# Kernel optimization log

Hardware: AMD Instinct MI355X
Metric: run time of the kernel (lower is better)

The kernel has to match this reference:

```python
import jax, jax.numpy as jnp
import numpy as np

D_IN, D_H, BATCH = 4096, 512, 8192


def _layernorm(x, g, b, eps=1e-5):
    mu = jnp.mean(x, axis=-1, keepdims=True)
    var = jnp.var(x, axis=-1, keepdims=True)
    return (x - mu) * jax.lax.rsqrt(var + eps) * g + b


def setup_inputs() -> dict:
    key = jax.random.key(0)
    ks = jax.random.split(key, 10)
    x = jax.random.normal(ks[0], (BATCH, D_IN), jnp.float32)
    h = jax.random.normal(ks[1], (BATCH, D_H), jnp.float32)
    s1 = 1.0 / np.sqrt(D_IN + D_H)
    W1 = jax.random.uniform(ks[2], (D_IN + D_H, D_H), jnp.float32, -s1, s1)
    b1 = jnp.zeros((D_H,), jnp.float32)
    ln1_g = jnp.ones((D_H,), jnp.float32)
    ln1_b = jnp.zeros((D_H,), jnp.float32)
    s2 = 1.0 / np.sqrt(D_H)
    W2 = jax.random.uniform(ks[3], (D_H, 3 * D_H), jnp.float32, -s2, s2)
    b2 = jnp.zeros((3 * D_H,), jnp.float32)
    base_tau = jnp.ones((D_H,), jnp.float32)  # time_constant_init = 1.0
    base_A = jax.random.normal(ks[4], (D_H, D_H), jnp.float32) * 0.1
    idx = jnp.arange(D_H)
    base_A = base_A.at[idx, idx].set(-0.5)
    base_B = jax.random.normal(ks[5], (D_IN, D_H), jnp.float32) * 0.1
    hn_g = jnp.ones((D_H,), jnp.float32)
    hn_b = jnp.zeros((D_H,), jnp.float32)
    return {"x": x, "h": h, "W1": W1, "b1": b1, "ln1_g": ln1_g, "ln1_b": ln1_b,
            "W2": W2, "b2": b2, "base_tau": base_tau, "base_A": base_A,
            "base_B": base_B, "hn_g": hn_g, "hn_b": hn_b}


def reference(x, h, W1, b1, ln1_g, ln1_b, W2, b2, base_tau, base_A, base_B, hn_g, hn_b):
    dt = 0.1
    # time_net hypernetwork
    xh = jnp.concatenate([x, h], axis=-1)                 # [B, D_IN+D_H]
    t = _layernorm(xh @ W1 + b1, ln1_g, ln1_b)
    t = jax.nn.gelu(t, approximate=False)
    params = t @ W2 + b2                                  # [B, 3*D_H]
    tau_s, A_s, B_s = jnp.split(params, 3, axis=-1)
    tau = base_tau * (jax.nn.sigmoid(tau_s) * 2.0)        # [B, D_H]
    A_row = 1.0 + 0.5 * jnp.tanh(A_s)                     # per-sample row scale of A
    B_col = 1.0 + 0.5 * jnp.tanh(B_s)                     # per-sample col scale of B
    # A[b] = base_A * A_row[b][:,None]; h @ A[b].T == (h @ base_A.T) * A_row[b]
    recurrent = (h @ base_A.T) * A_row                    # [B, D_H]
    # B[b] = base_B * B_col[b][None,:]; x @ B[b] == (x @ base_B) * B_col[b]
    input_term = (x @ base_B) * B_col                     # [B, D_H]
    dhdt = -h / (tau + 1e-8) + jnp.tanh(recurrent + input_term)
    new_h = _layernorm(h + dt * dhdt, hn_g, hn_b)
    return new_h
```

## Files before the change

kernel.cpp:

```cpp
#include <hip/hip_runtime.h>

#define BATCH 8192
#define DIN 4096
#define DH 512

typedef float f32x4 __attribute__((ext_vector_type(4)));
typedef float f32x2 __attribute__((ext_vector_type(2)));
typedef short s16x8 __attribute__((ext_vector_type(8)));
typedef unsigned short u16x2 __attribute__((ext_vector_type(2)));
typedef unsigned short u16x4 __attribute__((ext_vector_type(4)));
typedef unsigned short u16x8 __attribute__((ext_vector_type(8)));

static __device__ __forceinline__ unsigned short f2bf(float f) {
  unsigned int u = __float_as_uint(f);
  u += 0x7FFFu + ((u >> 16) & 1u);
  return (unsigned short)(u >> 16);
}
static __device__ __forceinline__ float bf2f(unsigned short s) {
  return __uint_as_float(((unsigned int)s) << 16);
}

typedef const __attribute__((address_space(1))) unsigned int* gas_ptr;
typedef __attribute__((address_space(3))) unsigned int* las_ptr;
static __device__ __forceinline__ void gl_lds16(const unsigned short* g, unsigned short* l) {
  __builtin_amdgcn_global_load_lds((gas_ptr)g, (las_ptr)l, 16, 0, 0);
}

__global__ __launch_bounds__(256) void cast_bf16_k(
    const float* __restrict__ in, unsigned short* __restrict__ out)
{
  const int i = (blockIdx.x * 256 + threadIdx.x) * 4;
  f32x4 v = *(const f32x4*)(in + i);
  u16x4 p = { f2bf(v[0]), f2bf(v[1]), f2bf(v[2]), f2bf(v[3]) };
  *(u16x4*)(out + i) = p;
}

__global__ __launch_bounds__(256) void transpose_bf16_k(
    const float* __restrict__ in, int R, int C,
    unsigned short* __restrict__ out, int ldo, int row_off)
{
  __shared__ float tl[32][33];
  const int tx = threadIdx.x, ty = threadIdx.y;
  const int c0 = blockIdx.x * 32, r0 = blockIdx.y * 32;
#pragma unroll
  for (int i = 0; i < 4; i++)
    tl[ty + 8 * i][tx] = in[(size_t)(r0 + ty + 8 * i) * C + c0 + tx];
  __syncthreads();
#pragma unroll
  for (int i = 0; i < 4; i++)
    out[(size_t)(row_off + c0 + ty + 8 * i) * ldo + r0 + tx] = f2bf(tl[tx][ty + 8 * i]);
}

__global__ __launch_bounds__(256) void zfill_k(
    unsigned short* __restrict__ base, int ld, int rows, int cols8)
{
  const int gid = blockIdx.x * 256 + threadIdx.x;
  const int row = gid / cols8;
  const int c = (gid % cols8) * 8;
  if (row < rows) {
    u16x8 z = { 0, 0, 0, 0, 0, 0, 0, 0 };
    *(u16x8*)(base + (size_t)row * ld + c) = z;
  }
}

template<int EPI>
static __device__ __forceinline__ void gemm_engine(
    const unsigned short* __restrict__ A0, int lda0, int K0,
    const unsigned short* __restrict__ A1, int lda1,
    const unsigned short* __restrict__ BT, int ldb,
    unsigned short* __restrict__ C0, int ldc,
    unsigned short* __restrict__ C1,
    const float* __restrict__ bias,
    const float* __restrict__ base_tau,
    int mb, int nb, int K,
    unsigned short* As, unsigned short* Bs)
{
  const int tid = threadIdx.x;
  const int lane = tid & 63;
  const int wid = tid >> 6;
  const int wm = (wid >> 1) * 64;
  const int wn = (wid & 1) * 64;
  const int srow = lane >> 2;
  const int scol = (lane & 3) * 8;
  const int fr = lane & 15;
  const int fk = (lane >> 4) * 8;
  const int NT = K / 32;

  f32x4 acc[4][4];
#pragma unroll
  for (int i = 0; i < 4; i++)
#pragma unroll
    for (int j = 0; j < 4; j++)
      acc[i][j] = (f32x4){ 0.f, 0.f, 0.f, 0.f };

  auto STAGE = [&](int buf, int t) {
    const int k0 = t * 32;
    const bool s0 = (k0 < K0);
    const unsigned short* Ab = s0 ? A0 : A1;
    const int ld = s0 ? lda0 : lda1;
    const int ko = (s0 ? k0 : k0 - K0) + scol;
    unsigned short* ab = As + buf * 4096 + (32 * wid) * 32;
    unsigned short* bb = Bs + buf * 4096 + (32 * wid) * 32;
#pragma unroll
    for (int c = 0; c < 2; c++) {
      const int r = 32 * wid + c * 16 + srow;
      gl_lds16(Ab + (size_t)(mb + r) * ld + ko, ab + c * 16 * 32);
      gl_lds16(BT + (size_t)(nb + r) * ldb + k0 + scol, bb + c * 16 * 32);
    }
  };

  STAGE(0, 0);
  STAGE(1, 1);
  asm volatile("s_waitcnt vmcnt(4)" ::: "memory");
  __builtin_amdgcn_s_barrier();

  int cur = 0, stg = 2;
  for (int t = 0; t < NT; t++) {
    if (t + 2 < NT) STAGE(stg, t + 2);

    const unsigned short* ar = As + cur * 4096;
    const unsigned short* br = Bs + cur * 4096;
    s16x8 af[4], bv[4];
#pragma unroll
    for (int mi = 0; mi < 4; mi++)
      af[mi] = *(const s16x8*)(ar + (wm + mi * 16 + fr) * 32 + fk);
#pragma unroll
    for (int ni = 0; ni < 4; ni++)
      bv[ni] = *(const s16x8*)(br + (wn + ni * 16 + fr) * 32 + fk);

    asm volatile("s_waitcnt lgkmcnt(0)" ::: "memory");
    __builtin_amdgcn_sched_barrier(0);

#pragma unroll
    for (int mi = 0; mi < 4; mi++)
#pragma unroll
      for (int ni = 0; ni < 4; ni++)
        acc[mi][ni] = __builtin_amdgcn_mfma_f32_16x16x32_bf16(
            af[mi], bv[ni], acc[mi][ni], 0, 0, 0);

    if (t + 1 < NT) {
      if (t + 2 < NT) asm volatile("s_waitcnt vmcnt(4)" ::: "memory");
      else            asm volatile("s_waitcnt vmcnt(0)" ::: "memory");
      __builtin_amdgcn_s_barrier();
    }
    cur = (cur == 2) ? 0 : cur + 1;
    stg = (stg == 2) ? 0 : stg + 1;
  }

  const int rb = (lane >> 4) * 4;
#pragma unroll
  for (int mi = 0; mi < 4; mi++) {
#pragma unroll
    for (int ni = 0; ni < 4; ni++) {
#pragma unroll
      for (int r = 0; r < 4; r++) {
        const int row = mb + wm + mi * 16 + rb + r;
        const int col = nb + wn + ni * 16 + fr;
        float v = acc[mi][ni][r];
        if (EPI == 3) {
          if (col < DH) C0[(size_t)row * DH + col] = f2bf(v + bias[col]);
          else          C1[(size_t)row * DH + (col - DH)] = f2bf(v);
        } else if (EPI == 2) {
          C0[(size_t)row * ldc + col] = f2bf(v);
        } else if (EPI == 1) {
          v += bias[col];
          if ((col >> 9) == 0) {
            const float s = 1.0f / (1.0f + expf(-v));
            v = 1.0f / (base_tau[col & (DH - 1)] * 2.0f * s + 1e-8f);
          } else {
            v = 1.0f + 0.5f * tanhf(v);
          }
          C0[(size_t)row * ldc + col] = f2bf(v);
        }
      }
    }
  }
}

__global__ __launch_bounds__(256) void fused_gemm_k(
    const unsigned short* __restrict__ xbf,
    const unsigned short* __restrict__ hbf,
    const unsigned short* __restrict__ BTcat,
    unsigned short* __restrict__ pre1,
    unsigned short* __restrict__ rawB,
    const float* __restrict__ b1)
{
  __shared__ unsigned short As[3 * 4096];
  __shared__ unsigned short Bs[3 * 4096];
  const int cpx = gridDim.x >> 3;
  const int virt = (blockIdx.x & 7) * cpx + (blockIdx.x >> 3);
  const int mb = (virt & 63) * 128;
  const int nb = (virt >> 6) * 128;
  gemm_engine<3>(xbf, DIN, DIN, hbf, DH, BTcat, DIN + DH,
                 pre1, DH, rawB, b1, nullptr, mb, nb, DIN + DH, As, Bs);
}

__global__ __launch_bounds__(256) void tail_gemm_k(
    const unsigned short* __restrict__ hbf,
    const unsigned short* __restrict__ Abf,
    const unsigned short* __restrict__ tbf,
    const unsigned short* __restrict__ W2T,
    unsigned short* __restrict__ rawA,
    unsigned short* __restrict__ scales,
    const float* __restrict__ b2,
    const float* __restrict__ base_tau)
{
  __shared__ unsigned short As[3 * 4096];
  __shared__ unsigned short Bs[3 * 4096];
  const int b = blockIdx.x;
  if (b < 768) {
    const int mb = (b & 63) * 128, nb = (b >> 6) * 128;
    gemm_engine<1>(tbf, DH, DH, nullptr, 0, W2T, DH,
                   scales, 3 * DH, nullptr, b2, base_tau, mb, nb, DH, As, Bs);
  } else {
    const int b2i = b - 768;
    const int mb = (b2i & 63) * 128, nb = (b2i >> 6) * 128;
    gemm_engine<2>(hbf, DH, DH, nullptr, 0, Abf, DH,
                   rawA, DH, nullptr, nullptr, nullptr, mb, nb, DH, As, Bs);
  }
}

__device__ __forceinline__ float block_sum256(float v, float* red) {
#pragma unroll
  for (int m = 32; m >= 1; m >>= 1) v += __shfl_xor(v, m, 64);
  __syncthreads();
  if ((threadIdx.x & 63) == 0) red[threadIdx.x >> 6] = v;
  __syncthreads();
  return red[0] + red[1] + red[2] + red[3];
}

__global__ __launch_bounds__(256) void ln_gelu_k(
    const unsigned short* __restrict__ pre,
    const float* __restrict__ g, const float* __restrict__ b,
    unsigned short* __restrict__ t)
{
  __shared__ float red[4];
  const int row = blockIdx.x;
  const int c = threadIdx.x * 2;
  const size_t ro = (size_t)row * DH;
  u16x2 raw = *(const u16x2*)(pre + ro + c);
  const float v0 = bf2f(raw[0]), v1 = bf2f(raw[1]);
  const float mu = block_sum256(v0 + v1, red) * (1.0f / DH);
  const float d0 = v0 - mu, d1 = v1 - mu;
  const float var = block_sum256(d0 * d0 + d1 * d1, red) * (1.0f / DH);
  const float inv = rsqrtf(var + 1e-5f);
  const float y0 = d0 * inv * g[c] + b[c];
  const float y1 = d1 * inv * g[c + 1] + b[c + 1];
  u16x2 o = { f2bf(0.5f * y0 * (1.0f + erff(y0 * 0.70710678118f))),
              f2bf(0.5f * y1 * (1.0f + erff(y1 * 0.70710678118f))) };
  *(u16x2*)(t + ro + c) = o;
}

__global__ __launch_bounds__(256) void final_k(
    const float* __restrict__ h,
    const unsigned short* __restrict__ rawA,
    const unsigned short* __restrict__ rawB,
    const unsigned short* __restrict__ scales,
    const float* __restrict__ hn_g, const float* __restrict__ hn_b,
    float* __restrict__ out)
{
  __shared__ float red[4];
  const int row = blockIdx.x;
  const int c = threadIdx.x * 2;
  const size_t ro = (size_t)row * DH;
  f32x2 hv = *(const f32x2*)(h + ro + c);
  u16x2 ra = *(const u16x2*)(rawA + ro + c);
  u16x2 rb = *(const u16x2*)(rawB + ro + c);
  const unsigned short* sc = scales + (size_t)row * (3 * DH);
  u16x2 ti  = *(const u16x2*)(sc + c);
  u16x2 arw = *(const u16x2*)(sc + DH + c);
  u16x2 bcl = *(const u16x2*)(sc + 2 * DH + c);
  const float u0 = hv[0] + 0.1f * (-hv[0] * bf2f(ti[0])
                 + tanhf(bf2f(ra[0]) * bf2f(arw[0]) + bf2f(rb[0]) * bf2f(bcl[0])));
  const float u1 = hv[1] + 0.1f * (-hv[1] * bf2f(ti[1])
                 + tanhf(bf2f(ra[1]) * bf2f(arw[1]) + bf2f(rb[1]) * bf2f(bcl[1])));
  const float mu = block_sum256(u0 + u1, red) * (1.0f / DH);
  const float d0 = u0 - mu, d1 = u1 - mu;
  const float var = block_sum256(d0 * d0 + d1 * d1, red) * (1.0f / DH);
  const float inv = rsqrtf(var + 1e-5f);
  f32x2 o = { d0 * inv * hn_g[c] + hn_b[c],
              d1 * inv * hn_g[c + 1] + hn_b[c + 1] };
  *(f32x2*)(out + ro + c) = o;
}

extern "C" void kernel_launch(void* const* d_in, const int* in_sizes, int n_in,
                              void* d_out, int out_size, void* d_ws, size_t ws_size,
                              hipStream_t stream)
{
  const float* x        = (const float*)d_in[0];
  const float* h        = (const float*)d_in[1];
  const float* W1       = (const float*)d_in[2];
  const float* b1       = (const float*)d_in[3];
  const float* ln1_g    = (const float*)d_in[4];
  const float* ln1_b    = (const float*)d_in[5];
  const float* W2       = (const float*)d_in[6];
  const float* b2       = (const float*)d_in[7];
  const float* base_tau = (const float*)d_in[8];
  const float* base_A   = (const float*)d_in[9];
  const float* base_B   = (const float*)d_in[10];
  const float* hn_g     = (const float*)d_in[11];
  const float* hn_b     = (const float*)d_in[12];

  const int KC = DIN + DH;
  char* w = (char*)d_ws;
  unsigned short* xbf    = (unsigned short*)(w);
  unsigned short* hbf    = (unsigned short*)(w + 67108864);
  unsigned short* BTcat  = (unsigned short*)(w + 75497472);
  unsigned short* tbf    = (unsigned short*)(w + 75497472);
  unsigned short* W2T    = (unsigned short*)(w + 84934656);
  unsigned short* Abf    = (unsigned short*)(w + 86507520);
  unsigned short* pre1   = (unsigned short*)(w + 87031808);
  unsigned short* rawA   = (unsigned short*)(w + 87031808);
  unsigned short* rawB   = (unsigned short*)(w + 95420416);
  unsigned short* scales = (unsigned short*)(w + 103809024);

  cast_bf16_k<<<DIN * BATCH / 1024, 256, 0, stream>>>(x, xbf);
  cast_bf16_k<<<DH * BATCH / 1024, 256, 0, stream>>>(h, hbf);
  cast_bf16_k<<<DH * DH / 1024, 256, 0, stream>>>(base_A, Abf);
  dim3 tb(32, 8);
  transpose_bf16_k<<<dim3(DH / 32, KC / 32), tb, 0, stream>>>(W1, KC, DH, BTcat, KC, 0);
  transpose_bf16_k<<<dim3(DH / 32, DIN / 32), tb, 0, stream>>>(base_B, DIN, DH, BTcat, KC, DH);
  zfill_k<<<128, 256, 0, stream>>>(BTcat + (size_t)DH * KC + DIN, KC, DH, DH / 8);
  transpose_bf16_k<<<dim3(3 * DH / 32, DH / 32), tb, 0, stream>>>(W2, DH, 3 * DH, W2T, DH, 0);

  fused_gemm_k<<<512, 256, 0, stream>>>(xbf, hbf, BTcat, pre1, rawB, b1);
  ln_gelu_k<<<BATCH, 256, 0, stream>>>(pre1, ln1_g, ln1_b, tbf);
  tail_gemm_k<<<1024, 256, 0, stream>>>(hbf, Abf, tbf, W2T, rawA, scales, b2, base_tau);
  final_k<<<BATCH, 256, 0, stream>>>(h, rawA, rawB, scales, hn_g, hn_b, (float*)d_out);
}
```

Baseline: 242.0 us.

## Deepen main GEMM pipeline to four stages and merge prep kernels into one launch

The main fused GEMM now keeps four LDS stages in flight instead of three. Its wait counts are generalised so up to two stages stay outstanding while compute runs, which should hide more global-load latency. Six small preprocessing launches (h cast, base_A cast, three transposes, zero fill) are merged into a single block-indexed kernel to cut launch overhead and tail gaps. The extra stage raises LDS per block to 64KB, which may lower occupancy.

After: 236.3 us. 2.4% less time.

```diff
diff --git a/kernel.cpp b/kernel.cpp
--- a/kernel.cpp
+++ b/kernel.cpp
@@ -35,13 +35,14 @@
   *(u16x4*)(out + i) = p;
 }
 
-__global__ __launch_bounds__(256) void transpose_bf16_k(
-    const float* __restrict__ in, int R, int C,
-    unsigned short* __restrict__ out, int ldo, int row_off)
-{
-  __shared__ float tl[32][33];
-  const int tx = threadIdx.x, ty = threadIdx.y;
-  const int c0 = blockIdx.x * 32, r0 = blockIdx.y * 32;
+static __device__ __forceinline__ void transpose_body(
+    const float* __restrict__ in, int C,
+    unsigned short* __restrict__ out, int ldo, int row_off,
+    int bx, int by, float (*tl)[33])
+{
+  const int tid = threadIdx.x;
+  const int tx = tid & 31, ty = tid >> 5;
+  const int c0 = bx * 32, r0 = by * 32;
 #pragma unroll
   for (int i = 0; i < 4; i++)
     tl[ty + 8 * i][tx] = in[(size_t)(r0 + ty + 8 * i) * C + c0 + tx];
@@ -51,19 +52,45 @@
     out[(size_t)(row_off + c0 + ty + 8 * i) * ldo + r0 + tx] = f2bf(tl[tx][ty + 8 * i]);
 }
 
-__global__ __launch_bounds__(256) void zfill_k(
-    unsigned short* __restrict__ base, int ld, int rows, int cols8)
-{
-  const int gid = blockIdx.x * 256 + threadIdx.x;
-  const int row = gid / cols8;
-  const int c = (gid % cols8) * 8;
-  if (row < rows) {
+__global__ __launch_bounds__(256) void prep_small_k(
+    const float* __restrict__ h, unsigned short* __restrict__ hbf,
+    const float* __restrict__ base_A, unsigned short* __restrict__ Abf,
+    const float* __restrict__ W1, const float* __restrict__ base_B,
+    unsigned short* __restrict__ BTcat,
+    const float* __restrict__ W2, unsigned short* __restrict__ W2T)
+{
+  __shared__ float tl[32][33];
+  const int b = blockIdx.x;
+  const int tid = threadIdx.x;
+  const int KC = DIN + DH;
+  if (b < 4096) {
+    const int i = (b * 256 + tid) * 4;
+    f32x4 v = *(const f32x4*)(h + i);
+    u16x4 p = { f2bf(v[0]), f2bf(v[1]), f2bf(v[2]), f2bf(v[3]) };
+    *(u16x4*)(hbf + i) = p;
+  } else if (b < 4352) {
+    const int i = ((b - 4096) * 256 + tid) * 4;
+    f32x4 v = *(const f32x4*)(base_A + i);
+    u16x4 p = { f2bf(v[0]), f2bf(v[1]), f2bf(v[2]), f2bf(v[3]) };
+    *(u16x4*)(Abf + i) = p;
+  } else if (b < 6656) {
+    const int bb = b - 4352;
+    transpose_body(W1, DH, BTcat, KC, 0, bb & 15, bb >> 4, tl);
+  } else if (b < 8704) {
+    const int bb = b - 6656;
+    transpose_body(base_B, DH, BTcat, KC, DH, bb & 15, bb >> 4, tl);
+  } else if (b < 8832) {
+    const int gid = (b - 8704) * 256 + tid;
+    const int row = gid >> 6, c = (gid & 63) * 8;
     u16x8 z = { 0, 0, 0, 0, 0, 0, 0, 0 };
-    *(u16x8*)(base + (size_t)row * ld + c) = z;
+    *(u16x8*)(BTcat + (size_t)(DH + row) * KC + DIN + c) = z;
+  } else {
+    const int bb = b - 8832;
+    transpose_body(W2, 3 * DH, W2T, DH, 0, bb % 48, bb / 48, tl);
   }
 }
 
-template<int EPI>
+template<int EPI, int DEPTH>
 static __device__ __forceinline__ void gemm_engine(
     const unsigned short* __restrict__ A0, int lda0, int K0,
     const unsigned short* __restrict__ A1, int lda1,
@@ -109,17 +136,17 @@
     }
   };
 
-  STAGE(0, 0);
-  STAGE(1, 1);
-  asm volatile("s_waitcnt vmcnt(4)" ::: "memory");
+#pragma unroll
+  for (int d = 0; d < DEPTH - 1; d++) STAGE(d, d);
+  if (DEPTH == 4) asm volatile("s_waitcnt vmcnt(8)" ::: "memory");
+  else            asm volatile("s_waitcnt vmcnt(4)" ::: "memory");
   __builtin_amdgcn_s_barrier();
 
-  int cur = 0, stg = 2;
   for (int t = 0; t < NT; t++) {
-    if (t + 2 < NT) STAGE(stg, t + 2);
-
-    const unsigned short* ar = As + cur * 4096;
-    const unsigned short* br = Bs + cur * 4096;
+    if (t + DEPTH - 1 < NT) STAGE((t + DEPTH - 1) % DEPTH, t + DEPTH - 1);
+
+    const unsigned short* ar = As + (t % DEPTH) * 4096;
+    const unsigned short* br = Bs + (t % DEPTH) * 4096;
     s16x8 af[4], bv[4];
 #pragma unroll
     for (int mi = 0; mi < 4; mi++)
@@ -139,12 +166,13 @@
             af[mi], bv[ni], acc[mi][ni], 0, 0, 0);
 
     if (t + 1 < NT) {
-      if (t + 2 < NT) asm volatile("s_waitcnt vmcnt(4)" ::: "memory");
-      else            asm volatile("s_waitcnt vmcnt(0)" ::: "memory");
+      const int rem = NT - 2 - t;
+      const int nw = (rem < DEPTH - 2) ? rem : DEPTH - 2;
+      if (nw >= 2)      asm volatile("s_waitcnt vmcnt(8)" ::: "memory");
+      else if (nw == 1) asm volatile("s_waitcnt vmcnt(4)" ::: "memory");
+      else              asm volatile("s_waitcnt vmcnt(0)" ::: "memory");
       __builtin_amdgcn_s_barrier();
     }
-    cur = (cur == 2) ? 0 : cur + 1;
-    stg = (stg == 2) ? 0 : stg + 1;
   }
 
   const int rb = (lane >> 4) * 4;
@@ -185,14 +213,14 @@
     unsigned short* __restrict__ rawB,
     const float* __restrict__ b1)
 {
-  __shared__ unsigned short As[3 * 4096];
-  __shared__ unsigned short Bs[3 * 4096];
+  __shared__ unsigned short As[4 * 4096];
+  __shared__ unsigned short Bs[4 * 4096];
   const int cpx = gridDim.x >> 3;
   const int virt = (blockIdx.x & 7) * cpx + (blockIdx.x >> 3);
   const int mb = (virt & 63) * 128;
   const int nb = (virt >> 6) * 128;
-  gemm_engine<3>(xbf, DIN, DIN, hbf, DH, BTcat, DIN + DH,
-                 pre1, DH, rawB, b1, nullptr, mb, nb, DIN + DH, As, Bs);
+  gemm_engine<3, 4>(xbf, DIN, DIN, hbf, DH, BTcat, DIN + DH,
+                    pre1, DH, rawB, b1, nullptr, mb, nb, DIN + DH, As, Bs);
 }
 
 __global__ __launch_bounds__(256) void tail_gemm_k(
@@ -210,13 +238,13 @@
   const int b = blockIdx.x;
   if (b < 768) {
     const int mb = (b & 63) * 128, nb = (b >> 6) * 128;
-    gemm_engine<1>(tbf, DH, DH, nullptr, 0, W2T, DH,
-                   scales, 3 * DH, nullptr, b2, base_tau, mb, nb, DH, As, Bs);
+    gemm_engine<1, 3>(tbf, DH, DH, nullptr, 0, W2T, DH,
+                      scales, 3 * DH, nullptr, b2, base_tau, mb, nb, DH, As, Bs);
   } else {
     const int b2i = b - 768;
     const int mb = (b2i & 63) * 128, nb = (b2i >> 6) * 128;
-    gemm_engine<2>(hbf, DH, DH, nullptr, 0, Abf, DH,
-                   rawA, DH, nullptr, nullptr, nullptr, mb, nb, DH, As, Bs);
+    gemm_engine<2, 3>(hbf, DH, DH, nullptr, 0, Abf, DH,
+                      rawA, DH, nullptr, nullptr, nullptr, mb, nb, DH, As, Bs);
   }
 }
 
@@ -301,7 +329,6 @@
   const float* hn_g     = (const float*)d_in[11];
   const float* hn_b     = (const float*)d_in[12];
 
-  const int KC = DIN + DH;
   char* w = (char*)d_ws;
   unsigned short* xbf    = (unsigned short*)(w);
   unsigned short* hbf    = (unsigned short*)(w + 67108864);
@@ -315,13 +342,7 @@
   unsigned short* scales = (unsigned short*)(w + 103809024);
 
   cast_bf16_k<<<DIN * BATCH / 1024, 256, 0, stream>>>(x, xbf);
-  cast_bf16_k<<<DH * BATCH / 1024, 256, 0, stream>>>(h, hbf);
-  cast_bf16_k<<<DH * DH / 1024, 256, 0, stream>>>(base_A, Abf);
-  dim3 tb(32, 8);
-  transpose_bf16_k<<<dim3(DH / 32, KC / 32), tb, 0, stream>>>(W1, KC, DH, BTcat, KC, 0);
-  transpose_bf16_k<<<dim3(DH / 32, DIN / 32), tb, 0, stream>>>(base_B, DIN, DH, BTcat, KC, DH);
-  zfill_k<<<128, 256, 0, stream>>>(BTcat + (size_t)DH * KC + DIN, KC, DH, DH / 8);
-  transpose_bf16_k<<<dim3(3 * DH / 32, DH / 32), tb, 0, stream>>>(W2, DH, 3 * DH, W2T, DH, 0);
+  prep_small_k<<<9600, 256, 0, stream>>>(h, hbf, base_A, Abf, W1, base_B, BTcat, W2, W2T);
 
   fused_gemm_k<<<512, 256, 0, stream>>>(xbf, hbf, BTcat, pre1, rawB, b1);
   ln_gelu_k<<<BATCH, 256, 0, stream>>>(pre1, ln1_g, ln1_b, tbf);
```
